# Kernel optimization log

Measured on AMD Instinct MI355X. Metric: run time of the kernel, lower is better.

The kernel has to match this reference:

```python
import jax, jax.numpy as jnp
import numpy as np

SEQ, BS, IN, HID, K = 256, 64, 512, 1024, 4


def setup_inputs() -> dict:
    key = jax.random.key(0)
    ks = jax.random.split(key, 6)
    s_ih = 1.0 / np.sqrt(HID)  # torch LSTM default uniform bound ~ 1/sqrt(hidden)
    x = jax.random.normal(ks[0], (SEQ, BS, IN), dtype=jnp.float32)
    h0 = jnp.zeros((1, BS, HID), dtype=jnp.float32)
    c0 = jnp.zeros((1, BS, HID), dtype=jnp.float32)
    coef = jax.random.uniform(ks[1], (SEQ, K), dtype=jnp.float32)
    Wih = jax.random.normal(ks[2], (K, 4 * HID, IN), dtype=jnp.float32) * s_ih
    Whh = jax.random.normal(ks[3], (K, 4 * HID, HID), dtype=jnp.float32) * s_ih
    bih = jax.random.normal(ks[4], (K, 4 * HID), dtype=jnp.float32) * s_ih
    bhh = jax.random.normal(ks[5], (K, 4 * HID), dtype=jnp.float32) * s_ih
    return {"x": x, "h0": h0, "c0": c0, "coef": coef,
            "Wih": Wih, "Whh": Whh, "bih": bih, "bhh": bhh}


def reference(x, h0, c0, coef, Wih, Whh, bih, bhh):
    """Mixture-of-Outputs LSTM over time.

    Per timestep t: run all K single-layer LSTM cells (PyTorch gate order
    i,f,g,o) on x[t] with the SHARED hidden state, then combine outputs,
    h, and c with softmax(coef[t]) weights. For a 1-layer LSTM single step,
    the output o equals the new h, so outputs[t] == combined h.
    """
    bias = (bih + bhh)[:, None, :]  # [K, 1, 4H]
    # Precompute input projections for all steps/experts: [SEQ, K, B, 4H]
    x_proj = jnp.einsum('tbi,kgi->tkbg', x, Wih) + bias[None]
    weights = jax.nn.softmax(coef[: x.shape[0]], axis=-1)  # [SEQ, K]

    def step(carry, inp):
        h, c = carry                      # [B, H] each
        xp_t, w = inp                     # [K, B, 4H], [K]
        gates = xp_t + jnp.einsum('bh,kgh->kbg', h, Whh)  # [K, B, 4H]
        i, f, g, o = jnp.split(gates, 4, axis=-1)
        i = jax.nn.sigmoid(i)
        f = jax.nn.sigmoid(f)
        g = jnp.tanh(g)
        o = jax.nn.sigmoid(o)
        c_k = f * c[None] + i * g         # [K, B, H]
        h_k = o * jnp.tanh(c_k)           # [K, B, H]
        h_new = jnp.einsum('k,kbh->bh', w, h_k)
        c_new = jnp.einsum('k,kbh->bh', w, c_k)
        return (h_new, c_new), h_new

    (h, c), outs = jax.lax.scan(step, (h0[0], c0[0]), (x_proj, weights))
    return outs, h[None], c[None]
```

## Files before the change

kernel.cpp:

```cpp
#include <hip/hip_runtime.h>

#define SEQ 256
#define BS 64
#define INF 512
#define HID 1024
#define KEXP 4
#define G4 4096
#define BH (BS * HID)

typedef __attribute__((ext_vector_type(8))) short s16x8;
typedef __attribute__((ext_vector_type(4))) float f32x4;

__device__ __forceinline__ short f2bf(float x) {
  unsigned u = __builtin_bit_cast(unsigned, x);
  u += 0x7fffu + ((u >> 16) & 1u);
  return (short)(u >> 16);
}

__device__ __forceinline__ float sigf(float x) {
  return 1.f / (1.f + __expf(-x));
}
__device__ __forceinline__ float tanhfast(float x) {
  return 2.f / (1.f + __expf(-2.f * x)) - 1.f;
}

__global__ void cvt_kernel(const float* __restrict__ s, short* __restrict__ d, int n4) {
  int stride = gridDim.x * blockDim.x;
  for (int i = blockIdx.x * blockDim.x + threadIdx.x; i < n4; i += stride) {
    float4 v = reinterpret_cast<const float4*>(s)[i];
    short4 o = make_short4(f2bf(v.x), f2bf(v.y), f2bf(v.z), f2bf(v.w));
    reinterpret_cast<short4*>(d)[i] = o;
  }
}

__global__ void prep_misc(const float* __restrict__ h0, const float* __restrict__ coef,
                          short* __restrict__ hseq, float* __restrict__ wtsbuf,
                          unsigned* __restrict__ bar) {
  int i = blockIdx.x * blockDim.x + threadIdx.x;
  hseq[i] = f2bf(h0[i]);
  if (i < 4096) bar[i] = 0u;
  if (i < SEQ) {
    float a = coef[i*4+0], b = coef[i*4+1], c = coef[i*4+2], d = coef[i*4+3];
    float m = fmaxf(fmaxf(a, b), fmaxf(c, d));
    float ea = __expf(a-m), eb = __expf(b-m), ec = __expf(c-m), ed = __expf(d-m);
    float inv = 1.f / (ea+eb+ec+ed);
    wtsbuf[i*4+0]=ea*inv; wtsbuf[i*4+1]=eb*inv; wtsbuf[i*4+2]=ec*inv; wtsbuf[i*4+3]=ed*inv;
  }
}

#define PHASE(c, bufofs)                                                         \
  { _Pragma("unroll")                                                            \
    for (int i = 0; i < 6; ++i) {                                                \
      if (((kk0 + i) >> 4) == (c)) {                                             \
        const int kbyte = ((kk0 + i - (c) * 16) << 6) + ((lane >> 4) << 4);      \
        _Pragma("unroll")                                                        \
        for (int m = 0; m < 4; ++m) {                                            \
          const int rowA = m * 16 + n16;                                         \
          const int addr = rowA * 1024 + (kbyte ^ ((rowA & 7) << 4));            \
          s16x8 af = *reinterpret_cast<const s16x8*>(sA + (bufofs) + (addr >> 1)); \
          acc[m][0] = __builtin_amdgcn_mfma_f32_16x16x32_bf16(af, wr[0][i], acc[m][0], 0, 0, 0); \
          acc[m][1] = __builtin_amdgcn_mfma_f32_16x16x32_bf16(af, wr[1][i], acc[m][1], 0, 0, 0); \
          acc[m][2] = __builtin_amdgcn_mfma_f32_16x16x32_bf16(af, wr[2][i], acc[m][2], 0, 0, 0); \
          acc[m][3] = __builtin_amdgcn_mfma_f32_16x16x32_bf16(af, wr[3][i], acc[m][3], 0, 0, 0); \
        }                                                                        \
      }                                                                          \
    }                                                                            \
  }

__global__ __launch_bounds__(512, 1) void moo_persistent(
    const float* __restrict__ Wih,
    const float* __restrict__ Whh,
    const float* __restrict__ bih,
    const float* __restrict__ bhh,
    const float* __restrict__ c0,
    const short* __restrict__ xb,
    const float* __restrict__ wtsbuf,
    short* __restrict__ hseq,
    unsigned* __restrict__ bar,
    float* __restrict__ outf)
{
  __shared__ short sA[65536];
  __shared__ float sG[64 * 68];
  __shared__ float sBias[64];

  const int tid = threadIdx.x;
  const int w = tid >> 6;
  const int lane = tid & 63;
  const int wg = blockIdx.x;
  const int n16 = lane & 15;
  const int kk0 = w * 6;

  s16x8 wr[4][6];
  {
    const int gate = n16 >> 2, j = lane & 3;
    #pragma unroll
    for (int f = 0; f < 4; ++f) {
      const int row = f * G4 + gate * HID + wg * 4 + j;
      #pragma unroll
      for (int i = 0; i < 6; ++i) {
        const int kk = kk0 + i;
        const float* src = (kk < 32)
            ? (Whh + (size_t)row * HID + (kk << 5) + ((lane >> 4) << 3))
            : (Wih + (size_t)row * INF + ((kk - 32) << 5) + ((lane >> 4) << 3));
        float4 a = reinterpret_cast<const float4*>(src)[0];
        float4 b = reinterpret_cast<const float4*>(src)[1];
        s16x8 o;
        o[0]=f2bf(a.x); o[1]=f2bf(a.y); o[2]=f2bf(a.z); o[3]=f2bf(a.w);
        o[4]=f2bf(b.x); o[5]=f2bf(b.y); o[6]=f2bf(b.z); o[7]=f2bf(b.w);
        wr[f][i] = o;
      }
    }
  }

  if (tid < 64) {
    const int e = tid >> 4, g = (tid >> 2) & 3, jj = tid & 3;
    const int idx = e * G4 + g * HID + wg * 4 + jj;
    sBias[tid] = bih[idx] + bhh[idx];
  }
  float cpriv[2] = {0.f, 0.f};
  if (tid < 128) {
    const int b = tid >> 1, p = (tid & 1) << 1;
    cpriv[0] = c0[b * HID + wg * 4 + p];
    cpriv[1] = c0[b * HID + wg * 4 + p + 1];
  }
  __syncthreads();

  auto stage = [&](int buf, int pc, const short* h_in, const short* xrow) {
    #pragma unroll
    for (int rr = 0; rr < 8; ++rr) {
      const int q = tid * 16 + rr * 8192;
      const int r2 = q >> 10;
      const int kb = (q & 1023) ^ ((r2 & 7) << 4);
      const short* g = (pc < 2)
          ? (h_in + r2 * 1024 + pc * 512 + (kb >> 1))
          : (xrow + r2 * 512 + (kb >> 1));
      short* l = sA + buf * 32768 + ((w * 1024 + rr * 8192) >> 1);
      __builtin_amdgcn_global_load_lds((const __attribute__((address_space(1))) void*)g,
                                       (__attribute__((address_space(3))) void*)l,
                                       16, 0, 0);
    }
  };

  for (int t = 0; t < SEQ; ++t) {
    const short* h_in = hseq + (size_t)t * BH;
    const short* xrow = xb + (size_t)t * (BS * INF);

    f32x4 acc[4][4];
    #pragma unroll
    for (int m = 0; m < 4; ++m)
      #pragma unroll
      for (int f = 0; f < 4; ++f)
        acc[m][f] = (f32x4){0.f, 0.f, 0.f, 0.f};

    stage(0, 0, h_in, xrow);
    __syncthreads();
    stage(1, 1, h_in, xrow);
    PHASE(0, 0)
    __syncthreads();
    stage(0, 2, h_in, xrow);
    PHASE(1, 32768)
    __syncthreads();
    PHASE(2, 0)

    #pragma unroll
    for (int p = 0; p < 8; ++p) {
      if (p) __syncthreads();
      #pragma unroll
      for (int m = 0; m < 4; ++m) {
        #pragma unroll
        for (int f = 0; f < 4; ++f) {
          if ((((m >> 1) << 2) | f) == ((w + p) & 7)) {
            const int idx = (f * 16 + n16) * 68 + m * 16 + ((lane >> 4) << 2);
            f32x4* ptr = reinterpret_cast<f32x4*>(&sG[idx]);
            if (p == 0) *ptr = acc[m][f];
            else { f32x4 v = *ptr; v += acc[m][f]; *ptr = v; }
          }
        }
      }
    }
    __syncthreads();

    if (tid < 128) {
      const int b = tid >> 1, p = (tid & 1) << 1;
      const int col = wg * 4 + p;
      float hnv[2], cnv[2];
      #pragma unroll
      for (int q = 0; q < 2; ++q) {
        const int jj = p + q;
        float hn = 0.f, cn = 0.f;
        #pragma unroll
        for (int e = 0; e < 4; ++e) {
          float iv = sG[(e * 16 +  0 + jj) * 68 + b] + sBias[e * 16 +  0 + jj];
          float fv = sG[(e * 16 +  4 + jj) * 68 + b] + sBias[e * 16 +  4 + jj];
          float gv = sG[(e * 16 +  8 + jj) * 68 + b] + sBias[e * 16 +  8 + jj];
          float ov = sG[(e * 16 + 12 + jj) * 68 + b] + sBias[e * 16 + 12 + jj];
          float is = sigf(iv), fs = sigf(fv), gs = tanhfast(gv), os = sigf(ov);
          float ck = fs * cpriv[q] + is * gs;
          float hk = os * tanhfast(ck);
          float wk = wtsbuf[t * 4 + e];
          hn += wk * hk;
          cn += wk * ck;
        }
        hnv[q] = hn; cnv[q] = cn; cpriv[q] = cn;
      }
      unsigned hv = (unsigned)(unsigned short)f2bf(hnv[0]) |
                    ((unsigned)(unsigned short)f2bf(hnv[1]) << 16);
      unsigned* hnext = (unsigned*)(hseq + (size_t)(t + 1) * BH);
      __hip_atomic_store(hnext + ((b * HID + col) >> 1), hv,
                         __ATOMIC_RELAXED, __HIP_MEMORY_SCOPE_AGENT);
      float2 ov2 = make_float2(hnv[0], hnv[1]);
      *reinterpret_cast<float2*>(outf + (size_t)t * BH + b * HID + col) = ov2;
      if (t == SEQ - 1) {
        *reinterpret_cast<float2*>(outf + (size_t)SEQ * BH + b * HID + col) = ov2;
        *reinterpret_cast<float2*>(outf + (size_t)SEQ * BH + BH + b * HID + col) =
            make_float2(cnv[0], cnv[1]);
      }
    }

    if (t < SEQ - 1) {
      __syncthreads();
      if (tid == 0) {
        const unsigned tgt = 16u * (unsigned)(t + 1);
        unsigned old = atomicAdd(&bar[(wg >> 4) * 64], 1u);
        if (old == tgt - 1u) {
          unsigned old2 = atomicAdd(&bar[1024], 1u);
          if (old2 == tgt - 1u)
            __hip_atomic_store(&bar[1040], (unsigned)(t + 1),
                               __ATOMIC_RELAXED, __HIP_MEMORY_SCOPE_AGENT);
        }
        while (__hip_atomic_load(&bar[1040], __ATOMIC_RELAXED,
                                 __HIP_MEMORY_SCOPE_AGENT) < (unsigned)(t + 1))
          __builtin_amdgcn_s_sleep(2);
      }
      __syncthreads();
    }
  }
}

extern "C" void kernel_launch(void* const* d_in, const int* in_sizes, int n_in,
                              void* d_out, int out_size, void* d_ws, size_t ws_size,
                              hipStream_t stream) {
  const float* x    = (const float*)d_in[0];
  const float* h0   = (const float*)d_in[1];
  const float* c0   = (const float*)d_in[2];
  const float* coef = (const float*)d_in[3];
  const float* Wih  = (const float*)d_in[4];
  const float* Whh  = (const float*)d_in[5];
  const float* bih  = (const float*)d_in[6];
  const float* bhh  = (const float*)d_in[7];
  float* out = (float*)d_out;
  char* ws = (char*)d_ws;

  short*    xb      = (short*)(ws);
  float*    wtsbuf  = (float*)(ws + 16777216);
  unsigned* bar     = (unsigned*)(ws + 16781312);
  short*    hseq    = (short*)(ws + 16797696);

  cvt_kernel<<<2048, 256, 0, stream>>>(x, xb, (SEQ * BS * INF) / 4);
  prep_misc<<<256, 256, 0, stream>>>(h0, coef, hseq, wtsbuf, bar);

  moo_persistent<<<256, 512, 0, stream>>>(Wih, Whh, bih, bhh, c0, xb, wtsbuf,
                                          hseq, bar, out);
}
```

Before: 3.575 ms.

## Prefetch next step's x tile during current step and split barrier release flags

Restructures the per-timestep staging so the x-projection chunk for step t+1 is loaded into LDS during step t, and the x phase runs first while the h halves load. This removes one barrier and one load-to-compute stall from the critical recurrent path. It also caches the softmax weights in LDS, uses nontemporal loads and stores for weights and outputs, and replicates the barrier release flag into 8 cache-line-separated slots to reduce polling contention. The launch bound is changed to allow 2 blocks, which may constrain registers for the 24 resident weight fragments.

```diff
diff --git a/kernel.cpp b/kernel.cpp
--- a/kernel.cpp
+++ b/kernel.cpp
@@ -10,6 +10,7 @@
 
 typedef __attribute__((ext_vector_type(8))) short s16x8;
 typedef __attribute__((ext_vector_type(4))) float f32x4;
+typedef __attribute__((ext_vector_type(2))) float f32x2;
 
 __device__ __forceinline__ short f2bf(float x) {
   unsigned u = __builtin_bit_cast(unsigned, x);
@@ -67,7 +68,7 @@
     }                                                                            \
   }
 
-__global__ __launch_bounds__(512, 1) void moo_persistent(
+__global__ __launch_bounds__(512, 2) void moo_persistent(
     const float* __restrict__ Wih,
     const float* __restrict__ Whh,
     const float* __restrict__ bih,
@@ -82,6 +83,7 @@
   __shared__ short sA[65536];
   __shared__ float sG[64 * 68];
   __shared__ float sBias[64];
+  __shared__ float sWts[SEQ * 4];
 
   const int tid = threadIdx.x;
   const int w = tid >> 6;
@@ -102,11 +104,11 @@
         const float* src = (kk < 32)
             ? (Whh + (size_t)row * HID + (kk << 5) + ((lane >> 4) << 3))
             : (Wih + (size_t)row * INF + ((kk - 32) << 5) + ((lane >> 4) << 3));
-        float4 a = reinterpret_cast<const float4*>(src)[0];
-        float4 b = reinterpret_cast<const float4*>(src)[1];
+        f32x4 a = __builtin_nontemporal_load(reinterpret_cast<const f32x4*>(src));
+        f32x4 b = __builtin_nontemporal_load(reinterpret_cast<const f32x4*>(src + 4));
         s16x8 o;
-        o[0]=f2bf(a.x); o[1]=f2bf(a.y); o[2]=f2bf(a.z); o[3]=f2bf(a.w);
-        o[4]=f2bf(b.x); o[5]=f2bf(b.y); o[6]=f2bf(b.z); o[7]=f2bf(b.w);
+        o[0]=f2bf(a[0]); o[1]=f2bf(a[1]); o[2]=f2bf(a[2]); o[3]=f2bf(a[3]);
+        o[4]=f2bf(b[0]); o[5]=f2bf(b[1]); o[6]=f2bf(b[2]); o[7]=f2bf(b[3]);
         wr[f][i] = o;
       }
     }
@@ -117,33 +119,36 @@
     const int idx = e * G4 + g * HID + wg * 4 + jj;
     sBias[tid] = bih[idx] + bhh[idx];
   }
+  sWts[tid] = wtsbuf[tid];
+  sWts[tid + 512] = wtsbuf[tid + 512];
   float cpriv[2] = {0.f, 0.f};
   if (tid < 128) {
     const int b = tid >> 1, p = (tid & 1) << 1;
     cpriv[0] = c0[b * HID + wg * 4 + p];
     cpriv[1] = c0[b * HID + wg * 4 + p + 1];
   }
-  __syncthreads();
-
-  auto stage = [&](int buf, int pc, const short* h_in, const short* xrow) {
+
+  auto stage = [&](int bufofs, const short* g0, int rs) {
     #pragma unroll
     for (int rr = 0; rr < 8; ++rr) {
       const int q = tid * 16 + rr * 8192;
       const int r2 = q >> 10;
       const int kb = (q & 1023) ^ ((r2 & 7) << 4);
-      const short* g = (pc < 2)
-          ? (h_in + r2 * 1024 + pc * 512 + (kb >> 1))
-          : (xrow + r2 * 512 + (kb >> 1));
-      short* l = sA + buf * 32768 + ((w * 1024 + rr * 8192) >> 1);
+      const short* g = g0 + r2 * rs + (kb >> 1);
+      short* l = sA + bufofs + ((w * 1024 + rr * 8192) >> 1);
       __builtin_amdgcn_global_load_lds((const __attribute__((address_space(1))) void*)g,
                                        (__attribute__((address_space(3))) void*)l,
                                        16, 0, 0);
     }
   };
 
+  stage(0, xb, 512);
+  __syncthreads();
+
   for (int t = 0; t < SEQ; ++t) {
     const short* h_in = hseq + (size_t)t * BH;
-    const short* xrow = xb + (size_t)t * (BS * INF);
+    const int XO = (t & 1) * 32768;
+    const int OO = XO ^ 32768;
 
     f32x4 acc[4][4];
     #pragma unroll
@@ -152,15 +157,15 @@
       for (int f = 0; f < 4; ++f)
         acc[m][f] = (f32x4){0.f, 0.f, 0.f, 0.f};
 
-    stage(0, 0, h_in, xrow);
+    stage(OO, h_in, 1024);
+    PHASE(2, XO)
     __syncthreads();
-    stage(1, 1, h_in, xrow);
-    PHASE(0, 0)
+    stage(XO, h_in + 512, 1024);
+    PHASE(0, OO)
     __syncthreads();
-    stage(0, 2, h_in, xrow);
-    PHASE(1, 32768)
-    __syncthreads();
-    PHASE(2, 0)
+    PHASE(1, XO)
+    if (t + 1 < SEQ)
+      stage(OO, xb + (size_t)(t + 1) * (BS * INF), 512);
 
     #pragma unroll
     for (int p = 0; p < 8; ++p) {
@@ -197,7 +202,7 @@
           float is = sigf(iv), fs = sigf(fv), gs = tanhfast(gv), os = sigf(ov);
           float ck = fs * cpriv[q] + is * gs;
           float hk = os * tanhfast(ck);
-          float wk = wtsbuf[t * 4 + e];
+          float wk = sWts[t * 4 + e];
           hn += wk * hk;
           cn += wk * ck;
         }
@@ -208,12 +213,15 @@
       unsigned* hnext = (unsigned*)(hseq + (size_t)(t + 1) * BH);
       __hip_atomic_store(hnext + ((b * HID + col) >> 1), hv,
                          __ATOMIC_RELAXED, __HIP_MEMORY_SCOPE_AGENT);
-      float2 ov2 = make_float2(hnv[0], hnv[1]);
-      *reinterpret_cast<float2*>(outf + (size_t)t * BH + b * HID + col) = ov2;
+      f32x2 ov2 = {hnv[0], hnv[1]};
+      __builtin_nontemporal_store(ov2,
+          reinterpret_cast<f32x2*>(outf + (size_t)t * BH + b * HID + col));
       if (t == SEQ - 1) {
-        *reinterpret_cast<float2*>(outf + (size_t)SEQ * BH + b * HID + col) = ov2;
-        *reinterpret_cast<float2*>(outf + (size_t)SEQ * BH + BH + b * HID + col) =
-            make_float2(cnv[0], cnv[1]);
+        f32x2 cv2 = {cnv[0], cnv[1]};
+        __builtin_nontemporal_store(ov2,
+            reinterpret_cast<f32x2*>(outf + (size_t)SEQ * BH + b * HID + col));
+        __builtin_nontemporal_store(cv2,
+            reinterpret_cast<f32x2*>(outf + (size_t)SEQ * BH + BH + b * HID + col));
       }
     }
 
@@ -224,11 +232,14 @@
         unsigned old = atomicAdd(&bar[(wg >> 4) * 64], 1u);
         if (old == tgt - 1u) {
           unsigned old2 = atomicAdd(&bar[1024], 1u);
-          if (old2 == tgt - 1u)
-            __hip_atomic_store(&bar[1040], (unsigned)(t + 1),
-                               __ATOMIC_RELAXED, __HIP_MEMORY_SCOPE_AGENT);
+          if (old2 == tgt - 1u) {
+            #pragma unroll
+            for (int xg = 0; xg < 8; ++xg)
+              __hip_atomic_store(&bar[1280 + xg * 16], (unsigned)(t + 1),
+                                 __ATOMIC_RELAXED, __HIP_MEMORY_SCOPE_AGENT);
+          }
         }
-        while (__hip_atomic_load(&bar[1040], __ATOMIC_RELAXED,
+        while (__hip_atomic_load(&bar[1280 + (wg & 7) * 16], __ATOMIC_RELAXED,
                                  __HIP_MEMORY_SCOPE_AGENT) < (unsigned)(t + 1))
           __builtin_amdgcn_s_sleep(2);
       }
```

Measured after the change: 3.022 ms. 15.5% less time.
